# Performance work log

Measured on AMD Instinct MI355X. Metric: run time of the kernel, lower is better.

The kernel has to match this reference:

```python
import jax, jax.numpy as jnp
import numpy as np

B, S, DIM, H, HD = 4, 1024, 1280, 16, 80
SCALE = HD ** -0.5
ROPE_THETA = 10000.0


def rotate_half(x):
    x1, x2 = jnp.split(x, 2, axis=-1)
    return jnp.concatenate([-x2, x1], axis=-1)


def setup_inputs() -> dict:
    key = jax.random.key(0)
    ks = jax.random.split(key, 5)
    x = jax.random.normal(ks[0], (B, S, DIM), dtype=jnp.float32)
    Wqkv = jax.random.normal(ks[1], (DIM, 3 * DIM), dtype=jnp.float32) * 0.02
    bqkv = jax.random.normal(ks[2], (3 * DIM,), dtype=jnp.float32) * 0.01
    Wproj = jax.random.normal(ks[3], (DIM, DIM), dtype=jnp.float32) * 0.02
    bproj = jax.random.normal(ks[4], (DIM,), dtype=jnp.float32) * 0.01
    # realistic rotary tables: (S, HD) with duplicated freq halves (matches rotate_half layout)
    inv_freq = 1.0 / (ROPE_THETA ** (jnp.arange(0, HD, 2, dtype=jnp.float32) / HD))
    freqs = jnp.outer(jnp.arange(S, dtype=jnp.float32), inv_freq)  # (S, HD/2)
    emb = jnp.concatenate([freqs, freqs], axis=-1)  # (S, HD)
    rope_cos = jnp.cos(emb)
    rope_sin = jnp.sin(emb)
    return {"x": x, "rope_cos": rope_cos, "rope_sin": rope_sin,
            "Wqkv": Wqkv, "bqkv": bqkv, "Wproj": Wproj, "bproj": bproj}


def reference(x, rope_cos, rope_sin, Wqkv, bqkv, Wproj, bproj):
    b, s, d = x.shape
    qkv = (x @ Wqkv + bqkv).reshape(b, s, 3, H, HD)
    q, k, v = qkv[:, :, 0], qkv[:, :, 1], qkv[:, :, 2]  # each (b, s, H, HD)
    cos = rope_cos[None, :, None, :]  # (1, s, 1, HD)
    sin = rope_sin[None, :, None, :]
    q = q * cos + rotate_half(q) * sin
    k = k * cos + rotate_half(k) * sin
    # SDPA with all-ones mask (full attention)
    scores = jnp.einsum("bqhd,bkhd->bhqk", q, k) * SCALE
    probs = jax.nn.softmax(scores, axis=-1)
    out = jnp.einsum("bhqk,bkhd->bqhd", probs, v).reshape(b, s, d)
    return out @ Wproj + bproj
```

## Files before the change

kernel.cpp:

```cpp
#include <hip/hip_runtime.h>
#include <math.h>

#define SCALE_F 0.11180339887498949f
#define HDP 96

typedef short  short8  __attribute__((ext_vector_type(8)));
typedef short  short4v __attribute__((ext_vector_type(4)));
typedef float  f32x4   __attribute__((ext_vector_type(4)));
typedef __bf16 bf16x8  __attribute__((ext_vector_type(8)));
typedef __bf16 bf16x4  __attribute__((ext_vector_type(4)));

__device__ __forceinline__ float bf2f(short s) {
  union { unsigned u; float f; } v;
  v.u = ((unsigned)(unsigned short)s) << 16;
  return v.f;
}
__device__ __forceinline__ short f2b(float f) {
  __bf16 h = (__bf16)f;
  return __builtin_bit_cast(short, h);
}
__device__ __forceinline__ bool probe_is_bf16(const unsigned* probe) {
  return (probe[1] & 0xFFFFu) != 0u;
}
__device__ __forceinline__ float load_scalar(const void* p, int i, bool isb) {
  return isb ? bf2f(((const short*)p)[i]) : ((const float*)p)[i];
}

__device__ __forceinline__ void gload_lds16(const short* g, short* l) {
  __builtin_amdgcn_global_load_lds(
      (const __attribute__((address_space(1))) void*)g,
      (__attribute__((address_space(3))) void*)l, 16, 0, 0);
}

template <typename V>
__device__ __forceinline__ auto mfma_try(V a, V b, f32x4 c, int)
    -> decltype(__builtin_amdgcn_mfma_f32_16x16x32_bf16(a, b, c, 0, 0, 0)) {
  return __builtin_amdgcn_mfma_f32_16x16x32_bf16(a, b, c, 0, 0, 0);
}
template <typename V>
__device__ __forceinline__ f32x4 mfma_try(V a, V b, f32x4 c, long) {
  return __builtin_amdgcn_mfma_f32_16x16x32_bf16(
      __builtin_bit_cast(bf16x8, a), __builtin_bit_cast(bf16x8, b), c, 0, 0, 0);
}
__device__ __forceinline__ f32x4 MFMA(short8 a, short8 b, f32x4 c) {
  return mfma_try(a, b, c, 0);
}

#if __has_builtin(__builtin_amdgcn_mfma_f32_16x16x16bf16_1k)
template <typename V>
__device__ __forceinline__ auto mfma16_try(V a, V b, f32x4 c, int)
    -> decltype(__builtin_amdgcn_mfma_f32_16x16x16bf16_1k(a, b, c, 0, 0, 0)) {
  return __builtin_amdgcn_mfma_f32_16x16x16bf16_1k(a, b, c, 0, 0, 0);
}
template <typename V>
__device__ __forceinline__ f32x4 mfma16_try(V a, V b, f32x4 c, long) {
  return __builtin_amdgcn_mfma_f32_16x16x16bf16_1k(
      __builtin_bit_cast(bf16x4, a), __builtin_bit_cast(bf16x4, b), c, 0, 0, 0);
}
__device__ __forceinline__ f32x4 MFMA16(short4v a, short4v b, f32x4 c) {
  return mfma16_try(a, b, c, 0);
}
#elif __has_builtin(__builtin_amdgcn_mfma_f32_16x16x16_bf16)
template <typename V>
__device__ __forceinline__ auto mfma16_try(V a, V b, f32x4 c, int)
    -> decltype(__builtin_amdgcn_mfma_f32_16x16x16_bf16(a, b, c, 0, 0, 0)) {
  return __builtin_amdgcn_mfma_f32_16x16x16_bf16(a, b, c, 0, 0, 0);
}
template <typename V>
__device__ __forceinline__ f32x4 mfma16_try(V a, V b, f32x4 c, long) {
  return __builtin_amdgcn_mfma_f32_16x16x16_bf16(
      __builtin_bit_cast(bf16x4, a), __builtin_bit_cast(bf16x4, b), c, 0, 0, 0);
}
__device__ __forceinline__ f32x4 MFMA16(short4v a, short4v b, f32x4 c) {
  return mfma16_try(a, b, c, 0);
}
#else
__device__ __forceinline__ f32x4 MFMA16(short4v a, short4v b, f32x4 c) {
  asm volatile("v_mfma_f32_16x16x16_bf16 %0, %1, %2, %0"
               : "+v"(c) : "v"(a), "v"(b));
  return c;
}
#endif

__global__ __launch_bounds__(256) void preproc_kernel(
    const void* __restrict__ xin, short* __restrict__ xout,
    const void* __restrict__ wqkv, short* __restrict__ wt1,
    const void* __restrict__ wproj, short* __restrict__ wt2,
    const unsigned* __restrict__ probe) {
  __shared__ float tile[32][33];
  bool isb = probe_is_bf16(probe);
  int bid = blockIdx.x;
  int t = threadIdx.x;
  if (bid < 2560) {
    size_t i = ((size_t)bid * 256 + t) * 8;
    if (isb) {
      *(short8*)&xout[i] = *(const short8*)((const short*)xin + i);
    } else {
      const float* f = (const float*)xin + i;
      float4 a0 = *(const float4*)f;
      float4 a1 = *(const float4*)(f + 4);
      short8 sv;
      sv[0] = f2b(a0.x); sv[1] = f2b(a0.y); sv[2] = f2b(a0.z); sv[3] = f2b(a0.w);
      sv[4] = f2b(a1.x); sv[5] = f2b(a1.y); sv[6] = f2b(a1.z); sv[7] = f2b(a1.w);
      *(short8*)&xout[i] = sv;
    }
    return;
  }
  int b2 = bid - 2560;
  const void* in; short* out; int R, C, bx, by;
  if (b2 < 4800) {
    in = wqkv; out = wt1; R = 1280; C = 3840;
    bx = b2 % 120; by = b2 / 120;
  } else {
    int b3 = b2 - 4800;
    in = wproj; out = wt2; R = 1280; C = 1280;
    bx = b3 % 40; by = b3 / 40;
  }
  int r = t >> 3, c4 = (t & 7) * 4;
  size_t idx = (size_t)(by * 32 + r) * C + bx * 32 + c4;
  if (isb) {
    short4v v = *(const short4v*)((const short*)in + idx);
    tile[r][c4 + 0] = bf2f(v[0]);
    tile[r][c4 + 1] = bf2f(v[1]);
    tile[r][c4 + 2] = bf2f(v[2]);
    tile[r][c4 + 3] = bf2f(v[3]);
  } else {
    float4 v = *(const float4*)((const float*)in + idx);
    tile[r][c4 + 0] = v.x;
    tile[r][c4 + 1] = v.y;
    tile[r][c4 + 2] = v.z;
    tile[r][c4 + 3] = v.w;
  }
  __syncthreads();
  int rr = t >> 3, k4 = (t & 7) * 4;
  short4v o;
  o[0] = f2b(tile[k4 + 0][rr]);
  o[1] = f2b(tile[k4 + 1][rr]);
  o[2] = f2b(tile[k4 + 2][rr]);
  o[3] = f2b(tile[k4 + 3][rr]);
  *(short4v*)&out[(size_t)(bx * 32 + rr) * R + by * 32 + k4] = o;
}

__global__ __launch_bounds__(512, 2) void gemm_qkv_kernel(
    const short* __restrict__ X, const short* __restrict__ Wt,
    const void* __restrict__ bias, const unsigned* __restrict__ probe,
    short* __restrict__ Qw, short* __restrict__ Kw, short* __restrict__ Vt) {
  const int K = 1280;
  __shared__ short Al[2][2][8192];
  __shared__ short Bl[2][2][8192];
  int t = threadIdx.x;
  int bm = blockIdx.x / 15, bn = blockIdx.x % 15;
  int m0 = bm * 256, n0 = bn * 256;
  int w = t >> 6, lane = t & 63;
  int quad = lane >> 4, l16 = lane & 15, l8 = l16 & 7;
  int arow = (w >> 2) * 64 + l16;
  int brow = (w & 3) * 32 + l16;
  int sr = t >> 3, t8s = t * 8;
  int sjs = (t & 7) ^ (sr & 7);
  int soff0 = ((quad ^ l8) * 8);
  int soff1 = (((4 + quad) ^ l8) * 8);
  f32x4 acc[2][2][4][2] = {};
  short8 afr[4][2];
  short8 bf0[2][2], bf1[2][2];

#define STAGE8(PTR, R0, KOFF, LP)                                            \
  {                                                                          \
    const short* g_ = (PTR) + (size_t)((R0) + sr) * 1280 + (KOFF) + sjs * 8; \
    gload_lds16(g_, (LP) + t8s);                                             \
    gload_lds16(g_ + 64 * 1280, (LP) + t8s + 4096);                          \
  }

#define READ_A(S, H)                                                         \
  {                                                                          \
    _Pragma("unroll") for (int mt = 0; mt < 4; mt++) {                       \
      int rp_ = (arow + mt * 16) * 64;                                       \
      afr[mt][0] = *(const short8*)&Al[S][H][rp_ + soff0];                   \
      afr[mt][1] = *(const short8*)&Al[S][H][rp_ + soff1];                   \
    }                                                                        \
  }
#define READ_B(DST, S, H)                                                    \
  {                                                                          \
    _Pragma("unroll") for (int nt = 0; nt < 2; nt++) {                       \
      int rp_ = (brow + nt * 16) * 64;                                       \
      DST[nt][0] = *(const short8*)&Bl[S][H][rp_ + soff0];                   \
      DST[nt][1] = *(const short8*)&Bl[S][H][rp_ + soff1];                   \
    }                                                                        \
  }
#define CLUST(QM, QN, BF, WAITI)                                             \
  {                                                                          \
    asm volatile("s_waitcnt lgkmcnt(" #WAITI ")" ::: "memory");              \
    __builtin_amdgcn_sched_barrier(0);                                       \
    _Pragma("unroll") for (int mt = 0; mt < 4; mt++)                         \
      _Pragma("unroll") for (int nt = 0; nt < 2; nt++) {                     \
        acc[QM][QN][mt][nt] = MFMA(afr[mt][0], BF[nt][0], acc[QM][QN][mt][nt]); \
        acc[QM][QN][mt][nt] = MFMA(afr[mt][1], BF[nt][1], acc[QM][QN][mt][nt]); \
      }                                                                      \
  }
#define BAR() __builtin_amdgcn_s_barrier()
#define VW4()                                                                \
  {                                                                          \
    asm volatile("s_waitcnt vmcnt(4)" ::: "memory");                         \
    __builtin_amdgcn_sched_barrier(0);                                       \
  }

  STAGE8(X,  m0,       0,  &Al[0][0][0]);
  STAGE8(X,  m0 + 128, 0,  &Al[0][1][0]);
  STAGE8(Wt, n0,       0,  &Bl[0][0][0]);
  STAGE8(Wt, n0 + 128, 0,  &Bl[0][1][0]);
  STAGE8(X,  m0,       64, &Al[1][0][0]);
  STAGE8(Wt, n0,       64, &Bl[1][0][0]);
  VW4();
  BAR();

  for (int i = 0; i < 10; i++) {
    int k1 = (2 * i + 1) * 64;
    int k2 = (2 * i + 2) * 64; if (k2 >= K) k2 = 0;
    int k3 = (2 * i + 3) * 64; if (k3 >= K) k3 = 0;
    READ_A(0, 0); READ_B(bf0, 0, 0); READ_B(bf1, 0, 1);
    STAGE8(X,  m0 + 128, k1, &Al[1][1][0]);
    STAGE8(Wt, n0 + 128, k1, &Bl[1][1][0]);
    __builtin_amdgcn_s_setprio(1);
    CLUST(0, 0, bf0, 4);
    CLUST(0, 1, bf1, 0);
    __builtin_amdgcn_s_setprio(0);
    BAR();
    READ_A(0, 1);
    STAGE8(X,  m0,       k2, &Al[0][0][0]);
    STAGE8(Wt, n0,       k2, &Bl[0][0][0]);
    __builtin_amdgcn_s_setprio(1);
    CLUST(1, 0, bf0, 0);
    CLUST(1, 1, bf1, 0);
    __builtin_amdgcn_s_setprio(0);
    VW4();
    BAR();
    READ_A(1, 0); READ_B(bf0, 1, 0); READ_B(bf1, 1, 1);
    STAGE8(X,  m0 + 128, k2, &Al[0][1][0]);
    STAGE8(Wt, n0 + 128, k2, &Bl[0][1][0]);
    __builtin_amdgcn_s_setprio(1);
    CLUST(0, 0, bf0, 4);
    CLUST(0, 1, bf1, 0);
    __builtin_amdgcn_s_setprio(0);
    BAR();
    READ_A(1, 1);
    STAGE8(X,  m0,       k3, &Al[1][0][0]);
    STAGE8(Wt, n0,       k3, &Bl[1][0][0]);
    __builtin_amdgcn_s_setprio(1);
    CLUST(1, 0, bf0, 0);
    CLUST(1, 1, bf1, 0);
    __builtin_amdgcn_s_setprio(0);
    VW4();
    BAR();
  }
  asm volatile("s_waitcnt vmcnt(0)" ::: "memory");
  __builtin_amdgcn_sched_barrier(0);

  bool isb = probe_is_bf16(probe);
  float bv[2][2];
#pragma unroll
  for (int qn = 0; qn < 2; qn++)
#pragma unroll
    for (int nt = 0; nt < 2; nt++)
      bv[qn][nt] =
          load_scalar(bias, n0 + qn * 128 + (w & 3) * 32 + nt * 16 + l16, isb);
#pragma unroll
  for (int qm = 0; qm < 2; qm++)
#pragma unroll
    for (int mt = 0; mt < 4; mt++) {
      int mbase = m0 + qm * 128 + (w >> 2) * 64 + mt * 16 + quad * 4;
      int b = mbase >> 10, sbase = mbase & 1023;
#pragma unroll
      for (int qn = 0; qn < 2; qn++)
#pragma unroll
        for (int nt = 0; nt < 2; nt++) {
          int n = n0 + qn * 128 + (w & 3) * 32 + nt * 16 + l16;
          int which = n / 1280;
          int rmod = n - which * 1280;
          int h = rmod / 80;
          int d = rmod - h * 80;
          int bh = b * 16 + h;
          if (which == 2) {
            short4v vv;
#pragma unroll
            for (int reg = 0; reg < 4; reg++)
              vv[reg] = f2b(acc[qm][qn][mt][nt][reg] + bv[qn][nt]);
            *(short4v*)&Vt[((size_t)bh * 80 + d) * 1024 + sbase] = vv;
          } else {
            short* dst = (which == 0 ? Qw : Kw);
#pragma unroll
            for (int reg = 0; reg < 4; reg++)
              dst[((size_t)bh * 1024 + sbase + reg) * HDP + d] =
                  f2b(acc[qm][qn][mt][nt][reg] + bv[qn][nt]);
          }
        }
    }
#undef STAGE8
#undef READ_A
#undef READ_B
#undef CLUST
#undef BAR
#undef VW4
}

__global__ __launch_bounds__(256) void rope_kernel(
    short* __restrict__ Qw, short* __restrict__ Kw,
    const void* __restrict__ cosb, const void* __restrict__ sinb,
    const unsigned* __restrict__ probe) {
  bool isb = probe_is_bf16(probe);
  int tg = blockIdx.x * 256 + threadIdx.x;
  int row_all = tg / 5;
  int p = tg - row_all * 5;
  int which = row_all >> 16;
  int r = row_all & 65535;
  int s = r & 1023;
  short* ptr = (which ? Kw : Qw) + (size_t)r * HDP;
  float scale = which ? 1.0f : SCALE_F;
  int d0 = p * 8, d1 = 40 + p * 8;
  short8 a = *(const short8*)&ptr[d0];
  short8 b = *(const short8*)&ptr[d1];
  float c0[8], s0[8], c1[8], s1[8];
  if (isb) {
    const short* cb = (const short*)cosb + s * 80;
    const short* sb = (const short*)sinb + s * 80;
    short8 vc0 = *(const short8*)&cb[d0];
    short8 vs0 = *(const short8*)&sb[d0];
    short8 vc1 = *(const short8*)&cb[d1];
    short8 vs1 = *(const short8*)&sb[d1];
#pragma unroll
    for (int j = 0; j < 8; j++) {
      c0[j] = bf2f(vc0[j]); s0[j] = bf2f(vs0[j]);
      c1[j] = bf2f(vc1[j]); s1[j] = bf2f(vs1[j]);
    }
  } else {
    const float* cb = (const float*)cosb + s * 80;
    const float* sb = (const float*)sinb + s * 80;
    float4 vc0a = *(const float4*)&cb[d0];
    float4 vc0b = *(const float4*)&cb[d0 + 4];
    float4 vs0a = *(const float4*)&sb[d0];
    float4 vs0b = *(const float4*)&sb[d0 + 4];
    float4 vc1a = *(const float4*)&cb[d1];
    float4 vc1b = *(const float4*)&cb[d1 + 4];
    float4 vs1a = *(const float4*)&sb[d1];
    float4 vs1b = *(const float4*)&sb[d1 + 4];
    c0[0] = vc0a.x; c0[1] = vc0a.y; c0[2] = vc0a.z; c0[3] = vc0a.w;
    c0[4] = vc0b.x; c0[5] = vc0b.y; c0[6] = vc0b.z; c0[7] = vc0b.w;
    s0[0] = vs0a.x; s0[1] = vs0a.y; s0[2] = vs0a.z; s0[3] = vs0a.w;
    s0[4] = vs0b.x; s0[5] = vs0b.y; s0[6] = vs0b.z; s0[7] = vs0b.w;
    c1[0] = vc1a.x; c1[1] = vc1a.y; c1[2] = vc1a.z; c1[3] = vc1a.w;
    c1[4] = vc1b.x; c1[5] = vc1b.y; c1[6] = vc1b.z; c1[7] = vc1b.w;
    s1[0] = vs1a.x; s1[1] = vs1a.y; s1[2] = vs1a.z; s1[3] = vs1a.w;
    s1[4] = vs1b.x; s1[5] = vs1b.y; s1[6] = vs1b.z; s1[7] = vs1b.w;
  }
  short8 o0, o1;
#pragma unroll
  for (int j = 0; j < 8; j++) {
    float av = bf2f(a[j]), bv = bf2f(b[j]);
    o0[j] = f2b((av * c0[j] - bv * s0[j]) * scale);
    o1[j] = f2b((bv * c1[j] + av * s1[j]) * scale);
  }
  *(short8*)&ptr[d0] = o0;
  *(short8*)&ptr[d1] = o1;
  if (p == 0) {
    short8 z = {};
    *(short8*)&ptr[80] = z;
    *(short8*)&ptr[88] = z;
  }
}

__global__ __launch_bounds__(512, 4) void attn_kernel(
    const short* __restrict__ Qw, const short* __restrict__ Kw,
    const short* __restrict__ Vt, short* __restrict__ out) {
  __shared__ short Klds[2][64 * 104];
  __shared__ short Vlds[2][80 * 72];
  int t = threadIdx.x;
  int w = t >> 6, lane = t & 63;
  int quad = lane >> 4, l16 = lane & 15;
  int bh = blockIdx.x & 63;
  int qt = blockIdx.x >> 6;
  int q0 = qt * 128;
  const short* Kb = Kw + (size_t)bh * 1024 * HDP;
  const short* Vb = Vt + (size_t)bh * 80 * 1024;

  short8 aq[3];
  {
    const short* qrow = Qw + ((size_t)bh * 1024 + q0 + w * 16 + l16) * HDP;
#pragma unroll
    for (int ks = 0; ks < 3; ks++)
      aq[ks] = *(const short8*)&qrow[ks * 32 + quad * 8];
  }

  short8 kreg[2], vreg[2];
#define PREFETCH(c)                                                        \
  {                                                                        \
    {                                                                      \
      int row = t / 12, col = (t % 12) * 8;                                \
      kreg[0] = *(const short8*)&Kb[(size_t)((c) + row) * HDP + col];      \
    }                                                                      \
    if (t < 256) {                                                         \
      int idx = 512 + t;                                                   \
      int row = idx / 12, col = (idx % 12) * 8;                            \
      kreg[1] = *(const short8*)&Kb[(size_t)((c) + row) * HDP + col];      \
    }                                                                      \
    {                                                                      \
      int d = t >> 3, s0 = (t & 7) * 8;                                    \
      vreg[0] = *(const short8*)&Vb[(size_t)d * 1024 + (c) + s0];          \
    }                                                                      \
    if (t < 128) {                                                         \
      int idx = 512 + t;                                                   \
      int d = idx >> 3, s0 = (idx & 7) * 8;                                \
      vreg[1] = *(const short8*)&Vb[(size_t)d * 1024 + (c) + s0];          \
    }                                                                      \
  }
#define STORE_LDS(P)                                                       \
  {                                                                        \
    {                                                                      \
      int row = t / 12, col = (t % 12) * 8;                                \
      *(short8*)&Klds[P][row * 104 + col] = kreg[0];                       \
    }                                                                      \
    if (t < 256) {                                                         \
      int idx = 512 + t;                                                   \
      int row = idx / 12, col = (idx % 12) * 8;                            \
      *(short8*)&Klds[P][row * 104 + col] = kreg[1];                       \
    }                                                                      \
    {                                                                      \
      int d = t >> 3, s0 = (t & 7) * 8;                                    \
      *(short8*)&Vlds[P][d * 72 + s0] = vreg[0];                           \
    }                                                                      \
    if (t < 128) {                                                         \
      int idx = 512 + t;                                                   \
      int d = idx >> 3, s0 = (idx & 7) * 8;                                \
      *(short8*)&Vlds[P][d * 72 + s0] = vreg[1];                           \
    }                                                                      \
  }

  PREFETCH(0);
  STORE_LDS(0);
  __syncthreads();

  f32x4 ofr[5] = {};
  float lsum = 0.f;

  int p = 0;
  for (int c = 0; c < 1024; c += 64, p ^= 1) {
    if (c + 64 < 1024) PREFETCH(c + 64);
    const short* Kl = &Klds[p][0];
    const short* Vl = &Vlds[p][0];
    f32x4 sf[4] = {};
#pragma unroll
    for (int nt = 0; nt < 4; nt++) {
      short8 bk0 = *(const short8*)&Kl[(nt * 16 + l16) * 104 + 0 * 32 + quad * 8];
      short8 bk1 = *(const short8*)&Kl[(nt * 16 + l16) * 104 + 1 * 32 + quad * 8];
      short8 bk2 = *(const short8*)&Kl[(nt * 16 + l16) * 104 + 2 * 32 + quad * 8];
      sf[nt] = MFMA(bk0, aq[0], sf[nt]);
      sf[nt] = MFMA(bk1, aq[1], sf[nt]);
      sf[nt] = MFMA(bk2, aq[2], sf[nt]);
    }
    short4v bp[4];
#pragma unroll
    for (int nt = 0; nt < 4; nt++) {
      float e0 = __expf(fminf(sf[nt][0], 30.f));
      float e1 = __expf(fminf(sf[nt][1], 30.f));
      float e2 = __expf(fminf(sf[nt][2], 30.f));
      float e3 = __expf(fminf(sf[nt][3], 30.f));
      lsum += (e0 + e1) + (e2 + e3);
      bp[nt][0] = f2b(e0); bp[nt][1] = f2b(e1);
      bp[nt][2] = f2b(e2); bp[nt][3] = f2b(e3);
    }
#pragma unroll
    for (int cc = 0; cc < 4; cc++)
#pragma unroll
      for (int nt5 = 0; nt5 < 5; nt5++) {
        short4v va =
            *(const short4v*)&Vl[(nt5 * 16 + l16) * 72 + cc * 16 + quad * 4];
        ofr[nt5] = MFMA16(va, bp[cc], ofr[nt5]);
      }
    if (c + 64 < 1024) {
      STORE_LDS(p ^ 1);
      __syncthreads();
    }
  }
  lsum += __shfl_xor(lsum, 16);
  lsum += __shfl_xor(lsum, 32);
  float inv = 1.f / lsum;
  int b = bh >> 4, h = bh & 15;
  int s = q0 + w * 16 + l16;
#pragma unroll
  for (int nt5 = 0; nt5 < 5; nt5++) {
    short4v o;
#pragma unroll
    for (int j = 0; j < 4; j++) o[j] = f2b(ofr[nt5][j] * inv);
    *(short4v*)&out[((size_t)(b * 1024 + s)) * 1280 + h * 80 + nt5 * 16 +
                    quad * 4] = o;
  }
}

__global__ __launch_bounds__(256) void gemm_proj_kernel(
    const short* __restrict__ A, const short* __restrict__ Wt,
    const void* __restrict__ bias, const unsigned* __restrict__ probe,
    float* __restrict__ out) {
  const int K = 1280;
  __shared__ short As[2][128 * 32];
  __shared__ short Bs[2][128 * 32];
  int t = threadIdx.x;
  int bm = blockIdx.x / 10;
  int bn = blockIdx.x % 10;
  int m0 = bm * 128, n0 = bn * 128;
  int w = t >> 6, lane = t & 63;
  int wm = w & 1, wn = w >> 1;
  int quad = lane >> 4, l16 = lane & 15;
  int row = t >> 2, ch = (t & 3) * 8, row2 = row + 64;
  int t8 = t * 8;
  const short* Ar  = A  + (size_t)(m0 + row)  * K + ch;
  const short* Ar2 = A  + (size_t)(m0 + row2) * K + ch;
  const short* Wr  = Wt + (size_t)(n0 + row)  * K + ch;
  const short* Wr2 = Wt + (size_t)(n0 + row2) * K + ch;
  f32x4 acc[4][4] = {};
  gload_lds16(Ar,  &As[0][t8]);
  gload_lds16(Ar2, &As[0][t8 + 2048]);
  gload_lds16(Wr,  &Bs[0][t8]);
  gload_lds16(Wr2, &Bs[0][t8 + 2048]);
  __syncthreads();
  int p = 0;
#define PROJ_COMPUTE(pp)                                                      \
  {                                                                           \
    short8 af[4], bfr[4];                                                     \
    _Pragma("unroll") for (int mt = 0; mt < 4; mt++)                          \
        af[mt] = *(const short8*)&As[pp][(wm * 64 + mt * 16 + l16) * 32 + quad * 8]; \
    _Pragma("unroll") for (int nt = 0; nt < 4; nt++)                          \
        bfr[nt] = *(const short8*)&Bs[pp][(wn * 64 + nt * 16 + l16) * 32 + quad * 8]; \
    _Pragma("unroll") for (int mt = 0; mt < 4; mt++)                          \
        _Pragma("unroll") for (int nt = 0; nt < 4; nt++)                      \
            acc[mt][nt] = MFMA(af[mt], bfr[nt], acc[mt][nt]);                 \
  }
  for (int k0 = 32; k0 < K; k0 += 32, p ^= 1) {
    gload_lds16(Ar + k0,  &As[p ^ 1][t8]);
    gload_lds16(Ar2 + k0, &As[p ^ 1][t8 + 2048]);
    gload_lds16(Wr + k0,  &Bs[p ^ 1][t8]);
    gload_lds16(Wr2 + k0, &Bs[p ^ 1][t8 + 2048]);
    PROJ_COMPUTE(p);
    __syncthreads();
  }
  PROJ_COMPUTE(p);
  bool isb = probe_is_bf16(probe);
  float bv[4];
#pragma unroll
  for (int nt = 0; nt < 4; nt++)
    bv[nt] = load_scalar(bias, n0 + wn * 64 + nt * 16 + l16, isb);
#pragma unroll
  for (int mt = 0; mt < 4; mt++) {
#pragma unroll
    for (int nt = 0; nt < 4; nt++) {
      int n = n0 + wn * 64 + nt * 16 + l16;
#pragma unroll
      for (int reg = 0; reg < 4; reg++) {
        int m = m0 + wm * 64 + mt * 16 + quad * 4 + reg;
        out[(size_t)m * 1280 + n] = acc[mt][nt][reg] + bv[nt];
      }
    }
  }
}

extern "C" void kernel_launch(void* const* d_in, const int* in_sizes, int n_in,
                              void* d_out, int out_size, void* d_ws, size_t ws_size,
                              hipStream_t stream) {
  const void* x        = d_in[0];
  const void* rope_cos = d_in[1];
  const void* rope_sin = d_in[2];
  const void* Wqkv     = d_in[3];
  const void* bqkv     = d_in[4];
  const void* Wproj    = d_in[5];
  const void* bproj    = d_in[6];
  const unsigned* probe = (const unsigned*)rope_cos;
  char* ws = (char*)d_ws;
  short* Wt1 = (short*)(ws + 0);
  short* Wt2 = (short*)(ws + 9830400);
  short* Qw  = (short*)(ws + 13107200);
  short* Kw  = (short*)(ws + 25690112);
  short* Vt  = (short*)(ws + 38273024);
  short* Xb  = (short*)(ws + 48758784);
  short* At  = (short*)(ws + 48758784);

  preproc_kernel<<<2560 + 6400, 256, 0, stream>>>(x, Xb, Wqkv, Wt1, Wproj, Wt2,
                                                  probe);
  gemm_qkv_kernel<<<240, 512, 0, stream>>>(Xb, Wt1, bqkv, probe, Qw, Kw, Vt);
  rope_kernel<<<2560, 256, 0, stream>>>(Qw, Kw, rope_cos, rope_sin, probe);
  attn_kernel<<<512, 512, 0, stream>>>(Qw, Kw, Vt, At);
  gemm_proj_kernel<<<32 * 10, 256, 0, stream>>>(At, Wt2, bproj, probe, (float*)d_out);
}
```

Before: 232.5 us.

## Give each attention wave two 16-row query tiles, halving block threads

The attention kernel now runs 256 threads per block (4 waves), and each wave handles 32 query rows as two 16-row tiles instead of 16 rows. Each K/V fragment read from LDS is reused for two MFMAs, which halves LDS read traffic per unit of compute and doubles MFMA independence. The cost is roughly double the accumulator and probability registers per thread. Fewer threads also means each thread issues more global-to-LDS copy work.

```diff
diff --git a/kernel.cpp b/kernel.cpp
--- a/kernel.cpp
+++ b/kernel.cpp
@@ -366,7 +366,7 @@
   }
 }
 
-__global__ __launch_bounds__(512, 4) void attn_kernel(
+__global__ __launch_bounds__(256, 2) void attn_kernel(
     const short* __restrict__ Qw, const short* __restrict__ Kw,
     const short* __restrict__ Vt, short* __restrict__ out) {
   __shared__ short Klds[2][64 * 104];
@@ -380,55 +380,46 @@
   const short* Kb = Kw + (size_t)bh * 1024 * HDP;
   const short* Vb = Vt + (size_t)bh * 80 * 1024;
 
-  short8 aq[3];
+  short8 aq0[3], aq1[3];
   {
-    const short* qrow = Qw + ((size_t)bh * 1024 + q0 + w * 16 + l16) * HDP;
-#pragma unroll
-    for (int ks = 0; ks < 3; ks++)
-      aq[ks] = *(const short8*)&qrow[ks * 32 + quad * 8];
-  }
-
-  short8 kreg[2], vreg[2];
+    const short* qr0 = Qw + ((size_t)bh * 1024 + q0 + w * 32 + l16) * HDP;
+    const short* qr1 = qr0 + 16 * HDP;
+#pragma unroll
+    for (int ks = 0; ks < 3; ks++) {
+      aq0[ks] = *(const short8*)&qr0[ks * 32 + quad * 8];
+      aq1[ks] = *(const short8*)&qr1[ks * 32 + quad * 8];
+    }
+  }
+
+  short8 kreg[3], vreg[3];
 #define PREFETCH(c)                                                        \
   {                                                                        \
-    {                                                                      \
-      int row = t / 12, col = (t % 12) * 8;                                \
-      kreg[0] = *(const short8*)&Kb[(size_t)((c) + row) * HDP + col];      \
+    _Pragma("unroll") for (int i = 0; i < 3; i++) {                        \
+      int idx = i * 256 + t;                                               \
+      int row = idx / 12, col = (idx % 12) * 8;                            \
+      kreg[i] = *(const short8*)&Kb[(size_t)((c) + row) * HDP + col];      \
     }                                                                      \
-    if (t < 256) {                                                         \
-      int idx = 512 + t;                                                   \
-      int row = idx / 12, col = (idx % 12) * 8;                            \
-      kreg[1] = *(const short8*)&Kb[(size_t)((c) + row) * HDP + col];      \
-    }                                                                      \
-    {                                                                      \
-      int d = t >> 3, s0 = (t & 7) * 8;                                    \
-      vreg[0] = *(const short8*)&Vb[(size_t)d * 1024 + (c) + s0];          \
-    }                                                                      \
-    if (t < 128) {                                                         \
-      int idx = 512 + t;                                                   \
-      int d = idx >> 3, s0 = (idx & 7) * 8;                                \
-      vreg[1] = *(const short8*)&Vb[(size_t)d * 1024 + (c) + s0];          \
+    _Pragma("unroll") for (int i = 0; i < 3; i++) {                        \
+      int idx = i * 256 + t;                                               \
+      if (idx < 640) {                                                     \
+        int d = idx >> 3, s0 = (idx & 7) * 8;                              \
+        vreg[i] = *(const short8*)&Vb[(size_t)d * 1024 + (c) + s0];        \
+      }                                                                    \
     }                                                                      \
   }
 #define STORE_LDS(P)                                                       \
   {                                                                        \
-    {                                                                      \
-      int row = t / 12, col = (t % 12) * 8;                                \
-      *(short8*)&Klds[P][row * 104 + col] = kreg[0];                       \
+    _Pragma("unroll") for (int i = 0; i < 3; i++) {                        \
+      int idx = i * 256 + t;                                               \
+      int row = idx / 12, col = (idx % 12) * 8;                            \
+      *(short8*)&Klds[P][row * 104 + col] = kreg[i];                       \
     }                                                                      \
-    if (t < 256) {                                                         \
-      int idx = 512 + t;                                                   \
-      int row = idx / 12, col = (idx % 12) * 8;                            \
-      *(short8*)&Klds[P][row * 104 + col] = kreg[1];                       \
-    }                                                                      \
-    {                                                                      \
-      int d = t >> 3, s0 = (t & 7) * 8;                                    \
-      *(short8*)&Vlds[P][d * 72 + s0] = vreg[0];                           \
-    }                                                                      \
-    if (t < 128) {                                                         \
-      int idx = 512 + t;                                                   \
-      int d = idx >> 3, s0 = (idx & 7) * 8;                                \
-      *(short8*)&Vlds[P][d * 72 + s0] = vreg[1];                           \
+    _Pragma("unroll") for (int i = 0; i < 3; i++) {                        \
+      int idx = i * 256 + t;                                               \
+      if (idx < 640) {                                                     \
+        int d = idx >> 3, s0 = (idx & 7) * 8;                              \
+        *(short8*)&Vlds[P][d * 72 + s0] = vreg[i];                         \
+      }                                                                    \
     }                                                                      \
   }
 
@@ -436,34 +427,44 @@
   STORE_LDS(0);
   __syncthreads();
 
-  f32x4 ofr[5] = {};
-  float lsum = 0.f;
+  f32x4 ofr0[5] = {}, ofr1[5] = {};
+  float lsum0 = 0.f, lsum1 = 0.f;
 
   int p = 0;
   for (int c = 0; c < 1024; c += 64, p ^= 1) {
     if (c + 64 < 1024) PREFETCH(c + 64);
     const short* Kl = &Klds[p][0];
     const short* Vl = &Vlds[p][0];
-    f32x4 sf[4] = {};
+    f32x4 sf0[4] = {}, sf1[4] = {};
 #pragma unroll
     for (int nt = 0; nt < 4; nt++) {
       short8 bk0 = *(const short8*)&Kl[(nt * 16 + l16) * 104 + 0 * 32 + quad * 8];
       short8 bk1 = *(const short8*)&Kl[(nt * 16 + l16) * 104 + 1 * 32 + quad * 8];
       short8 bk2 = *(const short8*)&Kl[(nt * 16 + l16) * 104 + 2 * 32 + quad * 8];
-      sf[nt] = MFMA(bk0, aq[0], sf[nt]);
-      sf[nt] = MFMA(bk1, aq[1], sf[nt]);
-      sf[nt] = MFMA(bk2, aq[2], sf[nt]);
-    }
-    short4v bp[4];
+      sf0[nt] = MFMA(bk0, aq0[0], sf0[nt]);
+      sf1[nt] = MFMA(bk0, aq1[0], sf1[nt]);
+      sf0[nt] = MFMA(bk1, aq0[1], sf0[nt]);
+      sf1[nt] = MFMA(bk1, aq1[1], sf1[nt]);
+      sf0[nt] = MFMA(bk2, aq0[2], sf0[nt]);
+      sf1[nt] = MFMA(bk2, aq1[2], sf1[nt]);
+    }
+    short4v bp0[4], bp1[4];
 #pragma unroll
     for (int nt = 0; nt < 4; nt++) {
-      float e0 = __expf(fminf(sf[nt][0], 30.f));
-      float e1 = __expf(fminf(sf[nt][1], 30.f));
-      float e2 = __expf(fminf(sf[nt][2], 30.f));
-      float e3 = __expf(fminf(sf[nt][3], 30.f));
-      lsum += (e0 + e1) + (e2 + e3);
-      bp[nt][0] = f2b(e0); bp[nt][1] = f2b(e1);
-      bp[nt][2] = f2b(e2); bp[nt][3] = f2b(e3);
+      float e0 = __expf(fminf(sf0[nt][0], 30.f));
+      float e1 = __expf(fminf(sf0[nt][1], 30.f));
+      float e2 = __expf(fminf(sf0[nt][2], 30.f));
+      float e3 = __expf(fminf(sf0[nt][3], 30.f));
+      lsum0 += (e0 + e1) + (e2 + e3);
+      bp0[nt][0] = f2b(e0); bp0[nt][1] = f2b(e1);
+      bp0[nt][2] = f2b(e2); bp0[nt][3] = f2b(e3);
+      float f0 = __expf(fminf(sf1[nt][0], 30.f));
+      float f1 = __expf(fminf(sf1[nt][1], 30.f));
+      float f2 = __expf(fminf(sf1[nt][2], 30.f));
+      float f3 = __expf(fminf(sf1[nt][3], 30.f));
+      lsum1 += (f0 + f1) + (f2 + f3);
+      bp1[nt][0] = f2b(f0); bp1[nt][1] = f2b(f1);
+      bp1[nt][2] = f2b(f2); bp1[nt][3] = f2b(f3);
     }
 #pragma unroll
     for (int cc = 0; cc < 4; cc++)
@@ -471,25 +472,34 @@
       for (int nt5 = 0; nt5 < 5; nt5++) {
         short4v va =
             *(const short4v*)&Vl[(nt5 * 16 + l16) * 72 + cc * 16 + quad * 4];
-        ofr[nt5] = MFMA16(va, bp[cc], ofr[nt5]);
+        ofr0[nt5] = MFMA16(va, bp0[cc], ofr0[nt5]);
+        ofr1[nt5] = MFMA16(va, bp1[cc], ofr1[nt5]);
       }
     if (c + 64 < 1024) {
       STORE_LDS(p ^ 1);
       __syncthreads();
     }
   }
-  lsum += __shfl_xor(lsum, 16);
-  lsum += __shfl_xor(lsum, 32);
-  float inv = 1.f / lsum;
+  lsum0 += __shfl_xor(lsum0, 16);
+  lsum0 += __shfl_xor(lsum0, 32);
+  lsum1 += __shfl_xor(lsum1, 16);
+  lsum1 += __shfl_xor(lsum1, 32);
+  float inv0 = 1.f / lsum0, inv1 = 1.f / lsum1;
   int b = bh >> 4, h = bh & 15;
-  int s = q0 + w * 16 + l16;
+  int s0r = q0 + w * 32 + l16;
+  int s1r = s0r + 16;
 #pragma unroll
   for (int nt5 = 0; nt5 < 5; nt5++) {
-    short4v o;
-#pragma unroll
-    for (int j = 0; j < 4; j++) o[j] = f2b(ofr[nt5][j] * inv);
-    *(short4v*)&out[((size_t)(b * 1024 + s)) * 1280 + h * 80 + nt5 * 16 +
-                    quad * 4] = o;
+    short4v o0, o1;
+#pragma unroll
+    for (int j = 0; j < 4; j++) {
+      o0[j] = f2b(ofr0[nt5][j] * inv0);
+      o1[j] = f2b(ofr1[nt5][j] * inv1);
+    }
+    *(short4v*)&out[((size_t)(b * 1024 + s0r)) * 1280 + h * 80 + nt5 * 16 +
+                    quad * 4] = o0;
+    *(short4v*)&out[((size_t)(b * 1024 + s1r)) * 1280 + h * 80 + nt5 * 16 +
+                    quad * 4] = o1;
   }
 }
 
@@ -583,6 +593,6 @@
                                                   probe);
   gemm_qkv_kernel<<<240, 512, 0, stream>>>(Xb, Wt1, bqkv, probe, Qw, Kw, Vt);
   rope_kernel<<<2560, 256, 0, stream>>>(Qw, Kw, rope_cos, rope_sin, probe);
-  attn_kernel<<<512, 512, 0, stream>>>(Qw, Kw, Vt, At);
+  attn_kernel<<<512, 256, 0, stream>>>(Qw, Kw, Vt, At);
   gemm_proj_kernel<<<32 * 10, 256, 0, stream>>>(At, Wt2, bproj, probe, (float*)d_out);
 }
```

Result: faster. 227.9 us (-2.0%).
